# Kernel optimization log

Hardware: AMD Instinct MI355X
Metric: run time of the kernel (lower is better)

Reference implementation:

```python
import jax, jax.numpy as jnp
import numpy as np
from math import sqrt

B, S, D_MODEL = 2, 2048, 1024
H = 16
ADIM = D_MODEL // H  # 64
K_REL = 16
N_PEMB = 2 * K_REL + 1  # 33, bidirectional rel-pos vocabulary


def setup_inputs() -> dict:
    key = jax.random.key(0)
    ks = jax.random.split(key, 8)
    sc = 0.02
    return {
        "iQ": jax.random.normal(ks[0], (B, S, D_MODEL), jnp.float32),
        "iK": jax.random.normal(ks[1], (B, S, D_MODEL), jnp.float32),
        "iV": jax.random.normal(ks[2], (B, S, D_MODEL), jnp.float32),
        "Wq": jax.random.normal(ks[3], (D_MODEL, D_MODEL), jnp.float32) * sc,
        "Wk": jax.random.normal(ks[4], (D_MODEL, D_MODEL), jnp.float32) * sc,
        "Wv": jax.random.normal(ks[5], (D_MODEL, D_MODEL), jnp.float32) * sc,
        "Wo": jax.random.normal(ks[6], (D_MODEL, D_MODEL), jnp.float32) * sc,
        "rel_pemb": jax.random.normal(ks[7], (N_PEMB, ADIM), jnp.float32) * sc,
    }


def reference(iQ, iK, iV, Wq, Wk, Wv, Wo, rel_pemb):
    b, nq, _ = iQ.shape
    seql = iK.shape[1]
    # projections -> [b, h, len, d]
    q = (iQ @ Wq).reshape(b, nq, H, ADIM).transpose(0, 2, 1, 3)
    k = (iK @ Wk).reshape(b, seql, H, ADIM).transpose(0, 2, 1, 3)
    v = (iV @ Wv).reshape(b, seql, H, ADIM).transpose(0, 2, 1, 3)
    # content scores: [b, h, nq, seql]
    scores = jnp.einsum("bhqd,bhsd->bhqs", q, k)
    # relative position bias: rel[i, j] = clamp(j - i, -K, K) + K
    pos = jnp.arange(seql)
    rel = jnp.clip(pos[None, :] - pos[:, None], -K_REL, K_REL) + K_REL
    rel = rel[seql - nq:, :]  # narrow to query rows: [nq, seql]
    e = rel_pemb[rel]  # [nq, seql, d]
    scores = scores + jnp.einsum("bhqd,qsd->bhqs", q, e)
    scores = scores / sqrt(ADIM)
    attn = jax.nn.softmax(scores, axis=-1)
    ctx = jnp.einsum("bhqs,bhsd->bqhd", attn, v).reshape(b, nq, H * ADIM)
    return ctx @ Wo
```

## Files before the change

kernel.cpp:

```cpp
#include <hip/hip_runtime.h>
#include <hip/hip_bf16.h>

#define BB 2
#define S 2048
#define DM 1024
#define H 16
#define ADIM 64
#define NP 33

typedef __bf16 bf16x8 __attribute__((ext_vector_type(8)));
typedef __bf16 bf16x4 __attribute__((ext_vector_type(4)));
typedef float f32x4 __attribute__((ext_vector_type(4)));

__device__ __forceinline__ void gload16(const void* g, void* l) {
  __builtin_amdgcn_global_load_lds(
      (__attribute__((address_space(1))) void*)(g),
      (__attribute__((address_space(3))) void*)(l), 16, 0, 0);
}

__global__ __launch_bounds__(256) void tobf16(
    const float* __restrict__ X0, const float* __restrict__ X1,
    const float* __restrict__ X2, __bf16* __restrict__ Y0,
    __bf16* __restrict__ Y1, __bf16* __restrict__ Y2) {
  const float* X; __bf16* Y;
  switch (blockIdx.z) {
    case 0: X = X0; Y = Y0; break;
    case 1: X = X1; Y = Y1; break;
    default: X = X2; Y = Y2; break;
  }
  size_t i = ((size_t)blockIdx.x * 256 + threadIdx.x) * 8;
  float4 a0 = *(const float4*)(X + i);
  float4 a1 = *(const float4*)(X + i + 4);
  bf16x8 v;
  v[0] = (__bf16)a0.x; v[1] = (__bf16)a0.y;
  v[2] = (__bf16)a0.z; v[3] = (__bf16)a0.w;
  v[4] = (__bf16)a1.x; v[5] = (__bf16)a1.y;
  v[6] = (__bf16)a1.z; v[7] = (__bf16)a1.w;
  *(bf16x8*)(Y + i) = v;
}

__global__ __launch_bounds__(256) void wtrans(
    const float* __restrict__ W0, const float* __restrict__ W1,
    const float* __restrict__ W2, __bf16* __restrict__ T0,
    __bf16* __restrict__ T1, __bf16* __restrict__ T2) {
  const float* W; __bf16* T;
  switch (blockIdx.z) {
    case 0: W = W0; T = T0; break;
    case 1: W = W1; T = T1; break;
    default: W = W2; T = T2; break;
  }
  __shared__ __bf16 tile[64][65];
  int j = threadIdx.x & 63, i0 = threadIdx.x >> 6;
  int n0 = blockIdx.x * 64, k0 = blockIdx.y * 64;
#pragma unroll
  for (int p = 0; p < 16; ++p) {
    int i = i0 + p * 4;
    tile[i][j] = (__bf16)W[(size_t)(k0 + i) * DM + n0 + j];
  }
  __syncthreads();
#pragma unroll
  for (int p = 0; p < 16; ++p) {
    int i = i0 + p * 4;
    T[(size_t)(n0 + i) * DM + k0 + j] = tile[j][i];
  }
}

#define LDK 40
template <bool A_FP32, int BN, typename CT>
__device__ __forceinline__ void gemm_body(const void* __restrict__ Av,
                                          const __bf16* __restrict__ BT,
                                          CT* __restrict__ C, int mode,
                                          int m0, int n0) {
  constexpr int NF = BN / 32;
  constexpr int BH = BN / 16;
  __shared__ __align__(16) __bf16 As[128 * LDK];
  __shared__ __align__(16) __bf16 Bs[BN * 32];
  int t = threadIdx.x;
  int w = t >> 6, lane = t & 63, l15 = lane & 15, quad = lane >> 4;
  int wm = w >> 1, wn = w & 1;
  constexpr int LA = A_FP32 ? LDK : 32;
  f32x4 acc[4][NF] = {};
  int lr = t >> 2;
  int lk = (t & 3) * 8;
  int r4 = lane >> 2;
  int c8 = (lane & 3) * 8;
  for (int k0 = 0; k0 < DM; k0 += 32) {
    if constexpr (A_FP32) {
#pragma unroll
      for (int rr = 0; rr < 2; ++rr) {
        int row = rr * 64 + lr;
        const float* src = (const float*)Av + (size_t)(m0 + row) * DM + k0 + lk;
        float4 a0 = *(const float4*)src;
        float4 a1 = *(const float4*)(src + 4);
        bf16x8 v;
        v[0] = (__bf16)a0.x; v[1] = (__bf16)a0.y;
        v[2] = (__bf16)a0.z; v[3] = (__bf16)a0.w;
        v[4] = (__bf16)a1.x; v[5] = (__bf16)a1.y;
        v[6] = (__bf16)a1.z; v[7] = (__bf16)a1.w;
        *(bf16x8*)&As[row * LDK + lk] = v;
      }
    } else {
#pragma unroll
      for (int q = 0; q < 2; ++q) {
        int half = w * 2 + q;
        gload16((const __bf16*)Av + (size_t)(m0 + half * 16 + r4) * DM + k0 + c8,
                &As[half * 512]);
      }
    }
#pragma unroll
    for (int q = 0; q < BH / 4; ++q) {
      int half = w * (BH / 4) + q;
      gload16(&BT[(size_t)(n0 + half * 16 + r4) * DM + k0 + c8],
              &Bs[half * 512]);
    }
    __syncthreads();
    bf16x8 af[4], bfr[NF];
#pragma unroll
    for (int mi = 0; mi < 4; ++mi)
      af[mi] = *(const bf16x8*)&As[(wm * 64 + mi * 16 + l15) * LA + quad * 8];
#pragma unroll
    for (int ni = 0; ni < NF; ++ni)
      bfr[ni] =
          *(const bf16x8*)&Bs[(wn * (BN / 2) + ni * 16 + l15) * 32 + quad * 8];
#pragma unroll
    for (int mi = 0; mi < 4; ++mi)
#pragma unroll
      for (int ni = 0; ni < NF; ++ni)
        acc[mi][ni] = __builtin_amdgcn_mfma_f32_16x16x32_bf16(
            af[mi], bfr[ni], acc[mi][ni], 0, 0, 0);
    __syncthreads();
  }
#pragma unroll
  for (int mi = 0; mi < 4; ++mi)
#pragma unroll
    for (int ni = 0; ni < NF; ++ni)
#pragma unroll
      for (int r = 0; r < 4; ++r) {
        int row = m0 + wm * 64 + mi * 16 + quad * 4 + r;
        int col = n0 + wn * (BN / 2) + ni * 16 + l15;
        CT v = (CT)acc[mi][ni][r];
        if (mode == 0) {
          C[(size_t)row * DM + col] = v;
        } else if (mode == 3) {
          int hh = row >> 6, dd = row & (ADIM - 1);
          int bb = col >> 11, ss = col & (S - 1);
          C[((size_t)(bb * H + hh) * ADIM + dd) * S + ss] = v;
        } else {
          int b = row >> 11, s = row & (S - 1);
          int h = col >> 6, d = col & (ADIM - 1);
          if (mode == 1)
            C[((size_t)(b * H + h) * S + s) * ADIM + d] = v;
          else
            C[((size_t)(b * H + h) * ADIM + d) * S + s] = v;
        }
      }
}

__global__ __launch_bounds__(256) void proj3(
    const float* __restrict__ iQ, const float* __restrict__ iK,
    const float* __restrict__ iV, const __bf16* __restrict__ WqT,
    const __bf16* __restrict__ WkT, const __bf16* __restrict__ WvT,
    __bf16* __restrict__ Qw, __bf16* __restrict__ Kw,
    __bf16* __restrict__ Vt) {
  const float* A; const __bf16* B; __bf16* C; int mode;
  switch (blockIdx.z) {
    case 0: A = iQ; B = WqT; C = Qw; mode = 1; break;
    case 1: A = iK; B = WkT; C = Kw; mode = 1; break;
    default: A = iV; B = WvT; C = Vt; mode = 2; break;
  }
  int i2 = blockIdx.x + (blockIdx.y << 3);
  int xcd = i2 & 7, slot = i2 >> 3;
  int m0 = (xcd + ((slot >> 3) << 3)) * 128;
  int n0 = (slot & 7) * 128;
  gemm_body<true, 128, __bf16>(A, B, C, mode, m0, n0);
}

__global__ __launch_bounds__(256) void proj3b(
    const __bf16* __restrict__ Qb, const __bf16* __restrict__ Kb,
    const __bf16* __restrict__ Vb, const __bf16* __restrict__ WqT,
    const __bf16* __restrict__ WkT, const __bf16* __restrict__ WvT,
    __bf16* __restrict__ Qw, __bf16* __restrict__ Kw,
    __bf16* __restrict__ Vt) {
  int i2 = blockIdx.x + (blockIdx.y << 3);
  if (blockIdx.z == 2) {
    int m0 = (i2 & 7) * 128;
    int n0 = (i2 >> 3) * 128;
    gemm_body<false, 128, __bf16>(WvT, Vb, Vt, 3, m0, n0);
  } else {
    const __bf16* A; const __bf16* B; __bf16* C;
    if (blockIdx.z == 0) { A = Qb; B = WqT; C = Qw; }
    else                 { A = Kb; B = WkT; C = Kw; }
    int xcd = i2 & 7, slot = i2 >> 3;
    int m0 = (xcd + ((slot >> 3) << 3)) * 128;
    int n0 = (slot & 7) * 128;
    gemm_body<false, 128, __bf16>(A, B, C, 1, m0, n0);
  }
}

__global__ __launch_bounds__(256) void gemm_final(
    const __bf16* __restrict__ ctx, const __bf16* __restrict__ WoT,
    float* __restrict__ out) {
  int i2 = blockIdx.x + (blockIdx.y << 4);
  int xcd = i2 & 7, slot = i2 >> 3;
  int m0 = ((xcd << 2) + (slot >> 4)) * 128;
  int n0 = (slot & 15) * 64;
  gemm_body<false, 64, float>(ctx, WoT, out, 0, m0, n0);
}

#define SWZ(row, sl) (((row) << 6) + ((((sl) ^ ((row) & 7))) << 3))
__global__ __launch_bounds__(256) void attn_flash(
    const __bf16* __restrict__ Qw, const __bf16* __restrict__ Kw,
    const __bf16* __restrict__ Vt, const float* __restrict__ pemb,
    __bf16* __restrict__ ctx) {
  int i = blockIdx.x + (blockIdx.y << 5);
  int a = i & 7, j = i >> 3;
  int bh = (a << 2) + (j >> 5);
  int q0 = (j & 31) * 64;
  int b = bh >> 4, h = bh & 15;
  int t = threadIdx.x, w = t >> 6, lane = t & 63, l15 = lane & 15,
      quad = lane >> 4;
  const __bf16* Qh = Qw + (size_t)bh * S * ADIM;
  const __bf16* Kh = Kw + (size_t)bh * S * ADIM;
  const __bf16* Vh = Vt + (size_t)bh * ADIM * S;

  __shared__ __align__(16) char smem[33280];
  __bf16* Ks = (__bf16*)smem;
  __bf16* Vs = (__bf16*)(smem + 8192);
  float* pband = (float*)(smem + 16384);
  __bf16* pbufw = (__bf16*)(smem + 25088 + w * 2048);
  __bf16* peb = (__bf16*)smem;

  for (int ii = t; ii < 48 * 64; ii += 256) {
    int r = ii >> 6, d = ii & 63;
    peb[r * 64 + d] = (r < NP) ? (__bf16)pemb[ii] : (__bf16)0.f;
  }

  int qa = q0 + w * 16 + l15;
  bf16x8 qf0 = *(const bf16x8*)&Qh[(size_t)qa * ADIM + quad * 8];
  bf16x8 qf1 = *(const bf16x8*)&Qh[(size_t)qa * ADIM + 32 + quad * 8];
  __syncthreads();

  {
    f32x4 pc[3] = {};
#pragma unroll
    for (int ni = 0; ni < 3; ++ni) {
      bf16x8 b0 = *(const bf16x8*)&peb[(ni * 16 + l15) * 64 + quad * 8];
      bf16x8 b1 = *(const bf16x8*)&peb[(ni * 16 + l15) * 64 + 32 + quad * 8];
      pc[ni] = __builtin_amdgcn_mfma_f32_16x16x32_bf16(qf0, b0, pc[ni], 0, 0, 0);
      pc[ni] = __builtin_amdgcn_mfma_f32_16x16x32_bf16(qf1, b1, pc[ni], 0, 0, 0);
    }
#pragma unroll
    for (int ni = 0; ni < 3; ++ni)
#pragma unroll
      for (int r = 0; r < 4; ++r) {
        int col = ni * 16 + l15;
        if (col < NP) pband[(w * 16 + quad * 4 + r) * 34 + col] = pc[ni][r];
      }
  }
  __syncthreads();

  int qg = q0 + w * 16 + l15;
  int qc = q0 + w * 16 + quad * 4;
  int qw0 = q0 + w * 16;
  const float* pbrow = pband + (w * 16 + l15) * 34;
  float lsum = 0.f;
  f32x4 o[4] = {};

  float pb0s = pbrow[0] * 0.125f;
  float pb32s = pbrow[32] * 0.125f;

  int srow = t >> 3;
  int sslot = t & 7;
  int scol = sslot * 8;
  bf16x8 k0r = *(const bf16x8*)&Kh[(size_t)srow * ADIM + scol];
  bf16x8 k1r = *(const bf16x8*)&Kh[(size_t)(32 + srow) * ADIM + scol];
  bf16x8 v0r = *(const bf16x8*)&Vh[(size_t)srow * S + scol];
  bf16x8 v1r = *(const bf16x8*)&Vh[(size_t)(32 + srow) * S + scol];

  for (int s0 = 0; s0 < S; s0 += 64) {
    __syncthreads();
    *(bf16x8*)&Ks[SWZ(srow, sslot)] = k0r;
    *(bf16x8*)&Ks[SWZ(32 + srow, sslot)] = k1r;
    *(bf16x8*)&Vs[SWZ(srow, sslot)] = v0r;
    *(bf16x8*)&Vs[SWZ(32 + srow, sslot)] = v1r;
    int sn = s0 + 64;
    if (sn < S) {
      k0r = *(const bf16x8*)&Kh[(size_t)(sn + srow) * ADIM + scol];
      k1r = *(const bf16x8*)&Kh[(size_t)(sn + 32 + srow) * ADIM + scol];
      v0r = *(const bf16x8*)&Vh[(size_t)srow * S + sn + scol];
      v1r = *(const bf16x8*)&Vh[(size_t)(32 + srow) * S + sn + scol];
    }
    __syncthreads();

    f32x4 c[4];
#pragma unroll
    for (int jj = 0; jj < 4; ++jj) {
      f32x4 cj = {};
      int krow = jj * 16 + l15;
      bf16x8 kb0 = *(const bf16x8*)&Ks[SWZ(krow, quad)];
      bf16x8 kb1 = *(const bf16x8*)&Ks[SWZ(krow, 4 + quad)];
      cj = __builtin_amdgcn_mfma_f32_16x16x32_bf16(kb0, qf0, cj, 0, 0, 0);
      cj = __builtin_amdgcn_mfma_f32_16x16x32_bf16(kb1, qf1, cj, 0, 0, 0);
      c[jj] = cj;
    }

    float pv[4][4];
    bool below = (s0 + 79 <= qw0);
    bool above = (s0 >= qw0 + 31);
    if (below || above) {
      float pb = below ? pb0s : pb32s;
#pragma unroll
      for (int jj = 0; jj < 4; ++jj)
#pragma unroll
        for (int r = 0; r < 4; ++r) {
          float e = __expf(__builtin_fmaf(c[jj][r], 0.125f, pb));
          lsum += e;
          pv[jj][r] = e;
        }
    } else {
#pragma unroll
      for (int jj = 0; jj < 4; ++jj)
#pragma unroll
        for (int r = 0; r < 4; ++r) {
          int sg = s0 + jj * 16 + quad * 4 + r;
          int i0 = sg - qg; i0 = i0 < -16 ? -16 : (i0 > 16 ? 16 : i0); i0 += 16;
          float e = __expf((c[jj][r] + pbrow[i0]) * 0.125f);
          lsum += e;
          pv[jj][r] = e;
        }
    }

#pragma unroll
    for (int jj = 0; jj < 4; ++jj) {
      bf16x4 pw;
      pw[0] = (__bf16)pv[jj][0]; pw[1] = (__bf16)pv[jj][1];
      pw[2] = (__bf16)pv[jj][2]; pw[3] = (__bf16)pv[jj][3];
      int sl = (2 * jj + (quad >> 1)) ^ (l15 & 7);
      *(bf16x4*)&pbufw[(l15 << 6) + (sl << 3) + (quad & 1) * 4] = pw;
    }
    bf16x8 pa0 = *(const bf16x8*)&pbufw[SWZ(l15, quad)];
    bf16x8 pa1 = *(const bf16x8*)&pbufw[SWZ(l15, 4 + quad)];

#pragma unroll
    for (int nt = 0; nt < 4; ++nt) {
      int vrow = nt * 16 + l15;
      bf16x8 vb0 = *(const bf16x8*)&Vs[SWZ(vrow, quad)];
      bf16x8 vb1 = *(const bf16x8*)&Vs[SWZ(vrow, 4 + quad)];
      o[nt] = __builtin_amdgcn_mfma_f32_16x16x32_bf16(pa0, vb0, o[nt], 0, 0, 0);
      o[nt] = __builtin_amdgcn_mfma_f32_16x16x32_bf16(pa1, vb1, o[nt], 0, 0, 0);
    }
  }

  lsum += __shfl_xor(lsum, 16, 64);
  lsum += __shfl_xor(lsum, 32, 64);
  float ls[4];
#pragma unroll
  for (int r = 0; r < 4; ++r) ls[r] = __shfl(lsum, quad * 4 + r, 64);
#pragma unroll
  for (int nt = 0; nt < 4; ++nt)
#pragma unroll
    for (int r = 0; r < 4; ++r) {
      int qq = qc + r;
      int d = nt * 16 + l15;
      ctx[(size_t)(b * S + qq) * DM + h * ADIM + d] =
          (__bf16)(o[nt][r] / ls[r]);
    }
}

extern "C" void kernel_launch(void* const* d_in, const int* in_sizes, int n_in,
                              void* d_out, int out_size, void* d_ws,
                              size_t ws_size, hipStream_t stream) {
  bool sizes_ok =
      (n_in == 8 && in_sizes[0] == BB * S * DM && in_sizes[1] == BB * S * DM &&
       in_sizes[2] == BB * S * DM && in_sizes[3] == DM * DM &&
       in_sizes[4] == DM * DM && in_sizes[5] == DM * DM &&
       in_sizes[6] == DM * DM && in_sizes[7] == NP * ADIM &&
       out_size == BB * S * DM);
  if (!sizes_ok) return;
  if (ws_size < 33ull * 1024 * 1024) return;

  const float* iQ = (const float*)d_in[0];
  const float* iK = (const float*)d_in[1];
  const float* iV = (const float*)d_in[2];
  const float* Wq = (const float*)d_in[3];
  const float* Wk = (const float*)d_in[4];
  const float* Wv = (const float*)d_in[5];
  const float* Wo = (const float*)d_in[6];
  const float* pemb = (const float*)d_in[7];

  char* w = (char*)d_ws;
  const size_t MB = 1024 * 1024;
  __bf16* Qw  = (__bf16*)(w + 0 * MB);
  __bf16* Kw  = (__bf16*)(w + 8 * MB);
  __bf16* Vt  = (__bf16*)(w + 16 * MB);
  __bf16* ctx = (__bf16*)(w + 24 * MB);
  __bf16* WqT = (__bf16*)(w + 24 * MB);
  __bf16* WkT = (__bf16*)(w + 26 * MB);
  __bf16* WvT = (__bf16*)(w + 28 * MB);
  __bf16* WoT = (__bf16*)(w + 0 * MB);

  wtrans<<<dim3(16, 16, 3), 256, 0, stream>>>(Wq, Wk, Wv, WqT, WkT, WvT);
  if (ws_size >= 56ull * 1024 * 1024) {
    __bf16* Qb = (__bf16*)(w + 32 * MB);
    __bf16* Kb = (__bf16*)(w + 40 * MB);
    __bf16* Vb = (__bf16*)(w + 48 * MB);
    tobf16<<<dim3(2048, 1, 3), 256, 0, stream>>>(iQ, iK, iV, Qb, Kb, Vb);
    proj3b<<<dim3(8, 32, 3), 256, 0, stream>>>(Qb, Kb, Vb, WqT, WkT, WvT,
                                               Qw, Kw, Vt);
  } else {
    proj3<<<dim3(8, 32, 3), 256, 0, stream>>>(iQ, iK, iV, WqT, WkT, WvT,
                                              Qw, Kw, Vt);
  }
  attn_flash<<<dim3(S / 64, BB * H), 256, 0, stream>>>(Qw, Kw, Vt, pemb, ctx);
  wtrans<<<dim3(16, 16, 1), 256, 0, stream>>>(Wo, Wo, Wo, WoT, WoT, WoT);
  gemm_final<<<dim3(16, 32), 256, 0, stream>>>(ctx, WoT, (float*)d_out);
}
```

Measured before the change: 241.9 us.

## Load V fragments directly from global memory and batch Wo transpose with others

The attention kernel no longer stages V tiles through shared memory. Each lane reads its MFMA B-operand fragments straight from the transposed V in global memory at the top of each iteration. This cuts LDS usage, which may allow more resident blocks, but every wave now issues its own uncoalesced-ish global loads with little prefetch distance. Separately, when the workspace is large enough, the Wo transpose is folded into the first weight-transpose launch, removing one kernel launch.

```diff
diff --git a/kernel.cpp b/kernel.cpp
--- a/kernel.cpp
+++ b/kernel.cpp
@@ -41,13 +41,15 @@
 
 __global__ __launch_bounds__(256) void wtrans(
     const float* __restrict__ W0, const float* __restrict__ W1,
-    const float* __restrict__ W2, __bf16* __restrict__ T0,
-    __bf16* __restrict__ T1, __bf16* __restrict__ T2) {
+    const float* __restrict__ W2, const float* __restrict__ W3,
+    __bf16* __restrict__ T0, __bf16* __restrict__ T1,
+    __bf16* __restrict__ T2, __bf16* __restrict__ T3) {
   const float* W; __bf16* T;
   switch (blockIdx.z) {
     case 0: W = W0; T = T0; break;
     case 1: W = W1; T = T1; break;
-    default: W = W2; T = T2; break;
+    case 2: W = W2; T = T2; break;
+    default: W = W3; T = T3; break;
   }
   __shared__ __bf16 tile[64][65];
   int j = threadIdx.x & 63, i0 = threadIdx.x >> 6;
@@ -223,11 +225,10 @@
   const __bf16* Kh = Kw + (size_t)bh * S * ADIM;
   const __bf16* Vh = Vt + (size_t)bh * ADIM * S;
 
-  __shared__ __align__(16) char smem[33280];
+  __shared__ __align__(16) char smem[25088];
   __bf16* Ks = (__bf16*)smem;
-  __bf16* Vs = (__bf16*)(smem + 8192);
-  float* pband = (float*)(smem + 16384);
-  __bf16* pbufw = (__bf16*)(smem + 25088 + w * 2048);
+  float* pband = (float*)(smem + 8192);
+  __bf16* pbufw = (__bf16*)(smem + 16896 + w * 2048);
   __bf16* peb = (__bf16*)smem;
 
   for (int ii = t; ii < 48 * 64; ii += 256) {
@@ -274,21 +275,22 @@
   int scol = sslot * 8;
   bf16x8 k0r = *(const bf16x8*)&Kh[(size_t)srow * ADIM + scol];
   bf16x8 k1r = *(const bf16x8*)&Kh[(size_t)(32 + srow) * ADIM + scol];
-  bf16x8 v0r = *(const bf16x8*)&Vh[(size_t)srow * S + scol];
-  bf16x8 v1r = *(const bf16x8*)&Vh[(size_t)(32 + srow) * S + scol];
 
   for (int s0 = 0; s0 < S; s0 += 64) {
+    bf16x8 vb0[4], vb1[4];
+#pragma unroll
+    for (int nt = 0; nt < 4; ++nt) {
+      int vrow = nt * 16 + l15;
+      vb0[nt] = *(const bf16x8*)&Vh[(size_t)vrow * S + s0 + quad * 8];
+      vb1[nt] = *(const bf16x8*)&Vh[(size_t)vrow * S + s0 + 32 + quad * 8];
+    }
     __syncthreads();
     *(bf16x8*)&Ks[SWZ(srow, sslot)] = k0r;
     *(bf16x8*)&Ks[SWZ(32 + srow, sslot)] = k1r;
-    *(bf16x8*)&Vs[SWZ(srow, sslot)] = v0r;
-    *(bf16x8*)&Vs[SWZ(32 + srow, sslot)] = v1r;
     int sn = s0 + 64;
     if (sn < S) {
       k0r = *(const bf16x8*)&Kh[(size_t)(sn + srow) * ADIM + scol];
       k1r = *(const bf16x8*)&Kh[(size_t)(sn + 32 + srow) * ADIM + scol];
-      v0r = *(const bf16x8*)&Vh[(size_t)srow * S + sn + scol];
-      v1r = *(const bf16x8*)&Vh[(size_t)(32 + srow) * S + sn + scol];
     }
     __syncthreads();
 
@@ -343,11 +345,8 @@
 
 #pragma unroll
     for (int nt = 0; nt < 4; ++nt) {
-      int vrow = nt * 16 + l15;
-      bf16x8 vb0 = *(const bf16x8*)&Vs[SWZ(vrow, quad)];
-      bf16x8 vb1 = *(const bf16x8*)&Vs[SWZ(vrow, 4 + quad)];
-      o[nt] = __builtin_amdgcn_mfma_f32_16x16x32_bf16(pa0, vb0, o[nt], 0, 0, 0);
-      o[nt] = __builtin_amdgcn_mfma_f32_16x16x32_bf16(pa1, vb1, o[nt], 0, 0, 0);
+      o[nt] = __builtin_amdgcn_mfma_f32_16x16x32_bf16(pa0, vb0[nt], o[nt], 0, 0, 0);
+      o[nt] = __builtin_amdgcn_mfma_f32_16x16x32_bf16(pa1, vb1[nt], o[nt], 0, 0, 0);
     }
   }
 
@@ -397,21 +396,34 @@
   __bf16* WqT = (__bf16*)(w + 24 * MB);
   __bf16* WkT = (__bf16*)(w + 26 * MB);
   __bf16* WvT = (__bf16*)(w + 28 * MB);
-  __bf16* WoT = (__bf16*)(w + 0 * MB);
-
-  wtrans<<<dim3(16, 16, 3), 256, 0, stream>>>(Wq, Wk, Wv, WqT, WkT, WvT);
-  if (ws_size >= 56ull * 1024 * 1024) {
+
+  bool big = ws_size >= 58ull * 1024 * 1024;
+  bool mid = ws_size >= 56ull * 1024 * 1024;
+  __bf16* WoT = big ? (__bf16*)(w + 56 * MB) : (__bf16*)(w + 0 * MB);
+
+  if (mid) {
     __bf16* Qb = (__bf16*)(w + 32 * MB);
     __bf16* Kb = (__bf16*)(w + 40 * MB);
     __bf16* Vb = (__bf16*)(w + 48 * MB);
+    wtrans<<<dim3(16, 16, big ? 4 : 3), 256, 0, stream>>>(
+        Wq, Wk, Wv, Wo, WqT, WkT, WvT, WoT);
     tobf16<<<dim3(2048, 1, 3), 256, 0, stream>>>(iQ, iK, iV, Qb, Kb, Vb);
     proj3b<<<dim3(8, 32, 3), 256, 0, stream>>>(Qb, Kb, Vb, WqT, WkT, WvT,
                                                Qw, Kw, Vt);
+    attn_flash<<<dim3(S / 64, BB * H), 256, 0, stream>>>(Qw, Kw, Vt, pemb,
+                                                         ctx);
+    if (!big)
+      wtrans<<<dim3(16, 16, 1), 256, 0, stream>>>(Wo, Wo, Wo, Wo,
+                                                  WoT, WoT, WoT, WoT);
   } else {
+    wtrans<<<dim3(16, 16, 3), 256, 0, stream>>>(Wq, Wk, Wv, Wq,
+                                                WqT, WkT, WvT, WqT);
     proj3<<<dim3(8, 32, 3), 256, 0, stream>>>(iQ, iK, iV, WqT, WkT, WvT,
                                               Qw, Kw, Vt);
-  }
-  attn_flash<<<dim3(S / 64, BB * H), 256, 0, stream>>>(Qw, Kw, Vt, pemb, ctx);
-  wtrans<<<dim3(16, 16, 1), 256, 0, stream>>>(Wo, Wo, Wo, WoT, WoT, WoT);
+    attn_flash<<<dim3(S / 64, BB * H), 256, 0, stream>>>(Qw, Kw, Vt, pemb,
+                                                         ctx);
+    wtrans<<<dim3(16, 16, 1), 256, 0, stream>>>(Wo, Wo, Wo, Wo,
+                                                WoT, WoT, WoT, WoT);
+  }
   gemm_final<<<dim3(16, 32), 256, 0, stream>>>(ctx, WoT, (float*)d_out);
 }
```

After: 308.7 us. +27.6%, slower.
